# Kernel tuning notes

Hardware: AMD Instinct MI355X
Metric: run time of the kernel (lower is better)

## Reference

```python
import jax, jax.numpy as jnp
import numpy as np

N = 100000
E = 800000
HID = 128
HEADS = 4
HD = HID // HEADS  # 32
EPS_SOFTMAX = 1e-16
LN_EPS = 1e-5


def setup_inputs() -> dict:
    key = jax.random.key(0)
    ks = jax.random.split(key, 12)
    s = 1.0 / np.sqrt(HID)
    x = jax.random.normal(ks[0], (N, HID), dtype=jnp.float32)
    edge_index = jax.random.randint(ks[1], (2, E), 0, N, dtype=jnp.int64)
    Wq = jax.random.normal(ks[2], (HID, HID), dtype=jnp.float32) * s
    bq = jnp.zeros((HID,), jnp.float32)
    Wk = jax.random.normal(ks[3], (HID, HID), dtype=jnp.float32) * s
    bk = jnp.zeros((HID,), jnp.float32)
    Wv = jax.random.normal(ks[4], (HID, HID), dtype=jnp.float32) * s
    bv = jnp.zeros((HID,), jnp.float32)
    Ws = jax.random.normal(ks[5], (HID, HID), dtype=jnp.float32) * s
    bs = jnp.zeros((HID,), jnp.float32)
    gamma = jnp.ones((HID,), jnp.float32)
    beta = jnp.zeros((HID,), jnp.float32)
    return {"x": x, "edge_index": edge_index, "Wq": Wq, "bq": bq,
            "Wk": Wk, "bk": bk, "Wv": Wv, "bv": bv,
            "Ws": Ws, "bs": bs, "gamma": gamma, "beta": beta}


def _transformer_conv(x, edge_index, Wq, bq, Wk, bk, Wv, bv, Ws, bs, gamma, beta):
    src = edge_index[0]  # message source j
    dst = edge_index[1]  # message target i
    # Projections -> [N, HEADS, HD]
    q = (x @ Wq + bq).reshape(N, HEADS, HD)
    k = (x @ Wk + bk).reshape(N, HEADS, HD)
    v = (x @ Wv + bv).reshape(N, HEADS, HD)
    # Edge-wise attention logits [E, HEADS]
    alpha = jnp.einsum('ehd,ehd->eh', q[dst], k[src]) / np.sqrt(HD).astype(np.float32)
    # Segment (per-destination) softmax, numerically stable
    amax = jax.ops.segment_max(alpha, dst, num_segments=N)  # [N, HEADS]
    amax = jnp.where(jnp.isfinite(amax), amax, 0.0)
    ex = jnp.exp(alpha - amax[dst])
    denom = jax.ops.segment_sum(ex, dst, num_segments=N)
    alpha = ex / (denom[dst] + EPS_SOFTMAX)
    # Weighted scatter-add of values
    out = jax.ops.segment_sum(alpha[:, :, None] * v[src], dst, num_segments=N)
    out = out.reshape(N, HID)
    # Root/skip connection (PyG root_weight=True, concat=True)
    out = out + x @ Ws + bs
    # LayerNorm
    mu = jnp.mean(out, axis=-1, keepdims=True)
    var = jnp.mean(jnp.square(out - mu), axis=-1, keepdims=True)
    return (out - mu) * jax.lax.rsqrt(var + LN_EPS) * gamma + beta


def reference(x, edge_index, Wq, bq, Wk, bk, Wv, bv, Ws, bs, gamma, beta):
    return _transformer_conv(x, edge_index, Wq, bq, Wk, bk, Wv, bv, Ws, bs, gamma, beta)
```

## Files before the change

kernel.cpp:

```cpp
#include <hip/hip_runtime.h>
#include <math.h>

#define N_NODES 100000
#define N_EDGES 800000
#define HID 128
#define HEADS 4
#define HD 32

#define KSCALE_L2E 0.2550348554422384f

#define PROJ_BLOCKS 391
#define FILL_BLOCKS 1563

typedef __attribute__((ext_vector_type(8))) short short8;
typedef __attribute__((ext_vector_type(4))) float f32x4;
typedef _Float16 h2 __attribute__((ext_vector_type(2)));
typedef __fp16 hf2 __attribute__((ext_vector_type(2)));

__device__ __forceinline__ unsigned int f2bf(float f) {
    unsigned int u = __float_as_uint(f);
    u += 0x7FFFu + ((u >> 16) & 1u);
    return (u >> 16) & 0xFFFFu;
}
__device__ __forceinline__ h2 u2h(unsigned int u) { return __builtin_bit_cast(h2, u); }
__device__ __forceinline__ unsigned int h2u(h2 h) { return __builtin_bit_cast(unsigned int, h); }
__device__ __forceinline__ unsigned int h2u(hf2 h) { return __builtin_bit_cast(unsigned int, h); }

__global__ __launch_bounds__(256) void prep(
    const float* __restrict__ Wq, const float* __restrict__ Wk,
    const float* __restrict__ Wv, const float* __restrict__ Ws,
    uint4* __restrict__ wtbf, const int* __restrict__ ei,
    int* __restrict__ deg)
{
    const int b = blockIdx.x;
    if (b < 32) {
        int idx = b * 256 + threadIdx.x;
        int m = idx >> 11, n = (idx >> 4) & 127, kc = idx & 15;
        const float* W = (m == 0) ? Wq : (m == 1) ? Wk : (m == 2) ? Wv : Ws;
        unsigned int h[8];
        #pragma unroll
        for (int j = 0; j < 8; ++j) h[j] = f2bf(W[(kc * 8 + j) * HID + n]);
        uint4 o;
        o.x = h[0] | (h[1] << 16);
        o.y = h[2] | (h[3] << 16);
        o.z = h[4] | (h[5] << 16);
        o.w = h[6] | (h[7] << 16);
        wtbf[idx] = o;
    } else {
        int e = (b - 32) * 256 + threadIdx.x;
        if (e < N_EDGES) atomicAdd(&deg[ei[N_EDGES + e]], 1);
    }
}

__global__ __launch_bounds__(256) void scan_local(const int* __restrict__ deg,
                                                  int* __restrict__ rowptr,
                                                  int* __restrict__ bsum)
{
    __shared__ int wsums[4];
    const int b = blockIdx.x, t = threadIdx.x, lane = t & 63, wid = t >> 6;
    const int base = b * 2048 + t * 8;
    int v[8], s = 0;
    #pragma unroll
    for (int j = 0; j < 8; ++j) {
        int i = base + j;
        v[j] = (i < N_NODES) ? deg[i] : 0;
        s += v[j];
    }
    const int tsum = s;
    int x = tsum;
    #pragma unroll
    for (int off = 1; off < 64; off <<= 1) {
        int t2 = __shfl_up(x, off);
        if (lane >= off) x += t2;
    }
    if (lane == 63) wsums[wid] = x;
    __syncthreads();
    int wpre = 0;
    #pragma unroll
    for (int ww = 0; ww < 4; ++ww) { if (ww < wid) wpre += wsums[ww]; }
    int run = wpre + x - tsum;
    #pragma unroll
    for (int j = 0; j < 8; ++j) {
        int i = base + j;
        if (i < N_NODES) rowptr[i] = run;
        run += v[j];
    }
    if (t == 0) bsum[b] = wsums[0] + wsums[1] + wsums[2] + wsums[3];
}

__global__ __launch_bounds__(256) void add_off(int* __restrict__ rowptr,
                                               const int* __restrict__ bsum)
{
    __shared__ int offs;
    const int t = threadIdx.x;
    const int tgt = blockIdx.x >> 3;
    if (t < 64) {
        int v = (t < tgt) ? bsum[t] : 0;
        #pragma unroll
        for (int off = 1; off < 64; off <<= 1) v += __shfl_xor(v, off);
        if (t == 0) offs = v;
    }
    __syncthreads();
    int i = blockIdx.x * 256 + t;
    if (i < N_NODES) rowptr[i] += offs;
    if (blockIdx.x == 0 && t == 0) rowptr[N_NODES] = N_EDGES;
}

__global__ __launch_bounds__(512) void fill_proj(
    const int* __restrict__ ei, const int* __restrict__ rowptr,
    int* __restrict__ deg, int* __restrict__ csr_src,
    const float* __restrict__ x, const uint4* __restrict__ wtbf,
    const float* __restrict__ bq, const float* __restrict__ bk,
    const float* __restrict__ bv, const float* __restrict__ bs,
    unsigned short* __restrict__ Qh, unsigned short* __restrict__ KVh,
    unsigned short* __restrict__ Sh)
{
    __shared__ uint4 wt[4096];

    if (blockIdx.x >= PROJ_BLOCKS) {
        int e = (blockIdx.x - PROJ_BLOCKS) * 512 + threadIdx.x;
        if (e < N_EDGES) {
            int src = ei[e], dst = ei[N_EDGES + e];
            int old = atomicSub(&deg[dst], 1);
            csr_src[rowptr[dst] + old - 1] = src;
        }
        return;
    }

    const int rb   = blockIdx.x * 256;
    const int tid  = threadIdx.x;
    const int lane = tid & 63;
    const int w    = tid >> 6;
    const int r    = lane & 15;
    const int kg   = lane >> 4;

    const int grow0 = rb + w * 32 + r;
    const int grow1 = grow0 + 16;
    short8 afr[2][4];
    #pragma unroll
    for (int rg = 0; rg < 2; ++rg) {
        const int grow = rg ? grow1 : grow0;
        #pragma unroll
        for (int s = 0; s < 4; ++s) {
            float4 a = make_float4(0.f, 0.f, 0.f, 0.f);
            float4 b = make_float4(0.f, 0.f, 0.f, 0.f);
            if (grow < N_NODES) {
                const float4* p = (const float4*)(x + (size_t)grow * HID + (s * 4 + kg) * 8);
                a = p[0]; b = p[1];
            }
            uint4 o;
            o.x = f2bf(a.x) | (f2bf(a.y) << 16);
            o.y = f2bf(a.z) | (f2bf(a.w) << 16);
            o.z = f2bf(b.x) | (f2bf(b.y) << 16);
            o.w = f2bf(b.z) | (f2bf(b.w) << 16);
            afr[rg][s] = *(short8*)&o;
        }
    }

    #pragma unroll
    for (int pair = 0; pair < 2; ++pair) {
        if (pair == 1) __syncthreads();
        #pragma unroll
        for (int it = 0; it < 8; ++it) {
            int cid = it * 512 + tid;
            int kc = cid & 15, n = (cid >> 4) & 127;
            wt[(cid & ~15) | (kc ^ (n & 7))] = wtbf[pair * 4096 + cid];
        }
        __syncthreads();

        #pragma unroll
        for (int mh = 0; mh < 2; ++mh) {
            const int m = pair * 2 + mh;
            const float* bias = (m == 0) ? bq : (m == 1) ? bk : (m == 2) ? bv : bs;
            const uint4* wtm = wt + mh * 2048;
            #pragma unroll
            for (int nt = 0; nt < 8; ++nt) {
                const int nrow = nt * 16 + r;
                const uint4* wrow = wtm + nrow * 16;
                f32x4 acc0, acc1;
                acc0[0]=0.f; acc0[1]=0.f; acc0[2]=0.f; acc0[3]=0.f;
                acc1[0]=0.f; acc1[1]=0.f; acc1[2]=0.f; acc1[3]=0.f;
                #pragma unroll
                for (int s = 0; s < 4; ++s) {
                    short8 bfr = *(const short8*)&wrow[(s * 4 + kg) ^ (nrow & 7)];
                    acc0 = __builtin_amdgcn_mfma_f32_16x16x32_bf16(bfr, afr[0][s], acc0, 0, 0, 0);
                    acc1 = __builtin_amdgcn_mfma_f32_16x16x32_bf16(bfr, afr[1][s], acc1, 0, 0, 0);
                }
                const int col = nt * 16 + kg * 4;
                float4 bi = *(const float4*)(bias + col);
                #pragma unroll
                for (int rg = 0; rg < 2; ++rg) {
                    const int grow = rg ? grow1 : grow0;
                    if (grow < N_NODES) {
                        f32x4 acc = rg ? acc1 : acc0;
                        float vx = acc[0] + bi.x, vy = acc[1] + bi.y;
                        float vz = acc[2] + bi.z, vw = acc[3] + bi.w;
                        if (m == 1) { vx *= KSCALE_L2E; vy *= KSCALE_L2E;
                                      vz *= KSCALE_L2E; vw *= KSCALE_L2E; }
                        uint2 pk;
                        pk.x = h2u(__builtin_amdgcn_cvt_pkrtz(vx, vy));
                        pk.y = h2u(__builtin_amdgcn_cvt_pkrtz(vz, vw));
                        unsigned short* dst =
                            (m == 0) ? (Qh + (size_t)grow * HID + col) :
                            (m == 1) ? (KVh + (size_t)grow * 256 + col) :
                            (m == 2) ? (KVh + (size_t)grow * 256 + 128 + col) :
                                       (Sh + (size_t)grow * HID + col);
                        *(uint2*)dst = pk;
                    }
                }
            }
        }
    }
}

__global__ __launch_bounds__(256) void node_attn(
    const int* __restrict__ rowptr, const int* __restrict__ csr_src,
    const unsigned short* __restrict__ Qh, const unsigned short* __restrict__ KVh,
    const unsigned short* __restrict__ Sh,
    const float* __restrict__ gamma, const float* __restrict__ beta,
    float* __restrict__ out)
{
    const int tid  = threadIdx.x;
    const int lane = tid & 63;
    const int node = blockIdx.x * 4 + (tid >> 6);
    if (node >= N_NODES) return;

    const int l8  = lane & 7;
    const int sl  = lane >> 3;
    const int j16 = l8 * 16;

    const int r0 = rowptr[node], r1 = rowptr[node + 1];

    const uint4* qp = (const uint4*)(Qh + (size_t)node * HID + j16);
    uint4 qa = qp[0], qb = qp[1];
    const h2 q0 = u2h(qa.x), q1 = u2h(qa.y), q2 = u2h(qa.z), q3 = u2h(qa.w);
    const h2 q4 = u2h(qb.x), q5 = u2h(qb.y), q6 = u2h(qb.z), q7 = u2h(qb.w);

    float den = 0.f;
    h2 ac0 = {0,0}, ac1 = {0,0}, ac2 = {0,0}, ac3 = {0,0};
    h2 ac4 = {0,0}, ac5 = {0,0}, ac6 = {0,0}, ac7 = {0,0};

    int p = r0 + sl;
    uint4 ka = {0,0,0,0}, kb = {0,0,0,0}, va = {0,0,0,0}, vb = {0,0,0,0};
    if (p < r1) {
        const unsigned short* base = KVh + (size_t)csr_src[p] * 256 + j16;
        ka = *(const uint4*)(base);
        kb = *(const uint4*)(base + 8);
        va = *(const uint4*)(base + 128);
        vb = *(const uint4*)(base + 136);
    }

    for (int it = r0; it < r1; it += 8) {
        uint4 kan = {0,0,0,0}, kbn = {0,0,0,0}, van = {0,0,0,0}, vbn = {0,0,0,0};
        const int pn = p + 8;
        if (pn < r1) {
            const unsigned short* base = KVh + (size_t)csr_src[pn] * 256 + j16;
            kan = *(const uint4*)(base);
            kbn = *(const uint4*)(base + 8);
            van = *(const uint4*)(base + 128);
            vbn = *(const uint4*)(base + 136);
        }

        h2 d = q0 * u2h(ka.x);
        d += q1 * u2h(ka.y);
        d += q2 * u2h(ka.z);
        d += q3 * u2h(ka.w);
        d += q4 * u2h(kb.x);
        d += q5 * u2h(kb.y);
        d += q6 * u2h(kb.z);
        d += q7 * u2h(kb.w);
        float t = (float)d.x + (float)d.y;
        t += __shfl_xor(t, 1);

        float e = (p < r1) ? __builtin_amdgcn_exp2f(t) : 0.f;
        den += e;
        _Float16 eh = (_Float16)e;
        h2 e2 = {eh, eh};
        ac0 += e2 * u2h(va.x);
        ac1 += e2 * u2h(va.y);
        ac2 += e2 * u2h(va.z);
        ac3 += e2 * u2h(va.w);
        ac4 += e2 * u2h(vb.x);
        ac5 += e2 * u2h(vb.y);
        ac6 += e2 * u2h(vb.z);
        ac7 += e2 * u2h(vb.w);

        p = pn; ka = kan; kb = kbn; va = van; vb = vbn;
    }

    #pragma unroll
    for (int msk = 8; msk <= 32; msk <<= 1) {
        den += __shfl_xor(den, msk);
        ac0 += u2h(__shfl_xor(h2u(ac0), msk));
        ac1 += u2h(__shfl_xor(h2u(ac1), msk));
        ac2 += u2h(__shfl_xor(h2u(ac2), msk));
        ac3 += u2h(__shfl_xor(h2u(ac3), msk));
        ac4 += u2h(__shfl_xor(h2u(ac4), msk));
        ac5 += u2h(__shfl_xor(h2u(ac5), msk));
        ac6 += u2h(__shfl_xor(h2u(ac6), msk));
        ac7 += u2h(__shfl_xor(h2u(ac7), msk));
    }

    float inv = 1.0f / (den + 1e-16f);
    const uint4* spp = (const uint4*)(Sh + (size_t)node * HID + j16);
    uint4 sa = spp[0], sb = spp[1];
    const h2 s0 = u2h(sa.x), s1 = u2h(sa.y), s2 = u2h(sa.z), s3 = u2h(sa.w);
    const h2 s4 = u2h(sb.x), s5 = u2h(sb.y), s6 = u2h(sb.z), s7 = u2h(sb.w);

    float o[16];
    o[0]  = (float)ac0.x * inv + (float)s0.x;  o[1]  = (float)ac0.y * inv + (float)s0.y;
    o[2]  = (float)ac1.x * inv + (float)s1.x;  o[3]  = (float)ac1.y * inv + (float)s1.y;
    o[4]  = (float)ac2.x * inv + (float)s2.x;  o[5]  = (float)ac2.y * inv + (float)s2.y;
    o[6]  = (float)ac3.x * inv + (float)s3.x;  o[7]  = (float)ac3.y * inv + (float)s3.y;
    o[8]  = (float)ac4.x * inv + (float)s4.x;  o[9]  = (float)ac4.y * inv + (float)s4.y;
    o[10] = (float)ac5.x * inv + (float)s5.x;  o[11] = (float)ac5.y * inv + (float)s5.y;
    o[12] = (float)ac6.x * inv + (float)s6.x;  o[13] = (float)ac6.y * inv + (float)s6.y;
    o[14] = (float)ac7.x * inv + (float)s7.x;  o[15] = (float)ac7.y * inv + (float)s7.y;

    float sum = 0.f, sq = 0.f;
    #pragma unroll
    for (int i = 0; i < 16; ++i) { sum += o[i]; sq += o[i] * o[i]; }
    #pragma unroll
    for (int off = 1; off < 8; off <<= 1) {
        sum += __shfl_xor(sum, off);
        sq  += __shfl_xor(sq, off);
    }
    float mean = sum * (1.0f / 128.0f);
    float var  = sq * (1.0f / 128.0f) - mean * mean;
    float rstd = rsqrtf(var + 1e-5f);

    if (sl == 0) {
        float* op = out + (size_t)node * HID + j16;
        #pragma unroll
        for (int c = 0; c < 4; ++c) {
            float4 g = *(const float4*)(gamma + j16 + c * 4);
            float4 b = *(const float4*)(beta + j16 + c * 4);
            float4 wv;
            wv.x = (o[c*4+0] - mean) * rstd * g.x + b.x;
            wv.y = (o[c*4+1] - mean) * rstd * g.y + b.y;
            wv.z = (o[c*4+2] - mean) * rstd * g.z + b.z;
            wv.w = (o[c*4+3] - mean) * rstd * g.w + b.w;
            *(float4*)(op + c * 4) = wv;
        }
    }
}

extern "C" void kernel_launch(void* const* d_in, const int* in_sizes, int n_in,
                              void* d_out, int out_size, void* d_ws, size_t ws_size,
                              hipStream_t stream) {
    const float* x  = (const float*)d_in[0];
    const int*   ei = (const int*)d_in[1];
    const float* Wq = (const float*)d_in[2];
    const float* bq = (const float*)d_in[3];
    const float* Wk = (const float*)d_in[4];
    const float* bk = (const float*)d_in[5];
    const float* Wv = (const float*)d_in[6];
    const float* bv = (const float*)d_in[7];
    const float* Ws = (const float*)d_in[8];
    const float* bs = (const float*)d_in[9];
    const float* gamma = (const float*)d_in[10];
    const float* beta  = (const float*)d_in[11];
    float* out = (float*)d_out;

    unsigned short* Qh  = (unsigned short*)d_ws;
    unsigned short* KVh = Qh + (size_t)N_NODES * HID;
    unsigned short* Sh  = KVh + (size_t)N_NODES * 256;
    uint4* wtbf  = (uint4*)(Sh + (size_t)N_NODES * HID);
    int* deg     = (int*)(wtbf + 4 * 128 * 16);
    int* rowptr  = deg + N_NODES;
    int* csr_src = rowptr + (N_NODES + 1);
    int* bsum    = csr_src + N_EDGES;

    hipMemsetAsync(deg, 0, N_NODES * sizeof(int), stream);

    const int eblk = (N_EDGES + 255) / 256;
    prep<<<32 + eblk, 256, 0, stream>>>(Wq, Wk, Wv, Ws, wtbf, ei, deg);

    const int nb = (N_NODES + 2047) / 2048;
    scan_local<<<nb, 256, 0, stream>>>(deg, rowptr, bsum);
    add_off<<<(N_NODES + 255) / 256, 256, 0, stream>>>(rowptr, bsum);

    fill_proj<<<PROJ_BLOCKS + FILL_BLOCKS, 512, 0, stream>>>(
        ei, rowptr, deg, csr_src, x, wtbf, bq, bk, bv, bs, Qh, KVh, Sh);

    node_attn<<<(N_NODES + 3) / 4, 256, 0, stream>>>(rowptr, csr_src, Qh, KVh, Sh,
                                                     gamma, beta, out);
}
```

Before: 197.0 us.

## Split fused CSR fill and projection into separate kernels, halve weight LDS

The combined fill_proj kernel is split into a standalone csr_fill kernel (256 threads per edge block) and a proj_mfma kernel. The projection kernel now stages one weight matrix at a time (32 KB of LDS instead of 64 KB), looping four times with a barrier between matrices. This is meant to raise occupancy for the projection blocks. The cost is an extra kernel launch, more barriers, and losing the overlap of edge scatter with the MFMA work inside a single grid.

```diff
diff --git a/kernel.cpp b/kernel.cpp
--- a/kernel.cpp
+++ b/kernel.cpp
@@ -8,9 +8,6 @@
 #define HD 32
 
 #define KSCALE_L2E 0.2550348554422384f
-
-#define PROJ_BLOCKS 391
-#define FILL_BLOCKS 1563
 
 typedef __attribute__((ext_vector_type(8))) short short8;
 typedef __attribute__((ext_vector_type(4))) float f32x4;
@@ -106,26 +103,26 @@
     if (blockIdx.x == 0 && t == 0) rowptr[N_NODES] = N_EDGES;
 }
 
-__global__ __launch_bounds__(512) void fill_proj(
-    const int* __restrict__ ei, const int* __restrict__ rowptr,
-    int* __restrict__ deg, int* __restrict__ csr_src,
+__global__ __launch_bounds__(256) void csr_fill(const int* __restrict__ ei,
+                                                const int* __restrict__ rowptr,
+                                                int* __restrict__ deg,
+                                                int* __restrict__ csr_src)
+{
+    int e = blockIdx.x * 256 + threadIdx.x;
+    if (e >= N_EDGES) return;
+    int src = ei[e], dst = ei[N_EDGES + e];
+    int old = atomicSub(&deg[dst], 1);
+    csr_src[rowptr[dst] + old - 1] = src;
+}
+
+__global__ __launch_bounds__(512) void proj_mfma(
     const float* __restrict__ x, const uint4* __restrict__ wtbf,
     const float* __restrict__ bq, const float* __restrict__ bk,
     const float* __restrict__ bv, const float* __restrict__ bs,
     unsigned short* __restrict__ Qh, unsigned short* __restrict__ KVh,
     unsigned short* __restrict__ Sh)
 {
-    __shared__ uint4 wt[4096];
-
-    if (blockIdx.x >= PROJ_BLOCKS) {
-        int e = (blockIdx.x - PROJ_BLOCKS) * 512 + threadIdx.x;
-        if (e < N_EDGES) {
-            int src = ei[e], dst = ei[N_EDGES + e];
-            int old = atomicSub(&deg[dst], 1);
-            csr_src[rowptr[dst] + old - 1] = src;
-        }
-        return;
-    }
+    __shared__ uint4 wt[2048];
 
     const int rb   = blockIdx.x * 256;
     const int tid  = threadIdx.x;
@@ -158,55 +155,50 @@
     }
 
     #pragma unroll
-    for (int pair = 0; pair < 2; ++pair) {
-        if (pair == 1) __syncthreads();
-        #pragma unroll
-        for (int it = 0; it < 8; ++it) {
+    for (int m = 0; m < 4; ++m) {
+        if (m > 0) __syncthreads();
+        #pragma unroll
+        for (int it = 0; it < 4; ++it) {
             int cid = it * 512 + tid;
             int kc = cid & 15, n = (cid >> 4) & 127;
-            wt[(cid & ~15) | (kc ^ (n & 7))] = wtbf[pair * 4096 + cid];
+            wt[(cid & ~15) | (kc ^ (n & 7))] = wtbf[m * 2048 + cid];
         }
         __syncthreads();
 
-        #pragma unroll
-        for (int mh = 0; mh < 2; ++mh) {
-            const int m = pair * 2 + mh;
-            const float* bias = (m == 0) ? bq : (m == 1) ? bk : (m == 2) ? bv : bs;
-            const uint4* wtm = wt + mh * 2048;
+        const float* bias = (m == 0) ? bq : (m == 1) ? bk : (m == 2) ? bv : bs;
+        #pragma unroll
+        for (int nt = 0; nt < 8; ++nt) {
+            const int nrow = nt * 16 + r;
+            const uint4* wrow = wt + nrow * 16;
+            f32x4 acc0, acc1;
+            acc0[0]=0.f; acc0[1]=0.f; acc0[2]=0.f; acc0[3]=0.f;
+            acc1[0]=0.f; acc1[1]=0.f; acc1[2]=0.f; acc1[3]=0.f;
             #pragma unroll
-            for (int nt = 0; nt < 8; ++nt) {
-                const int nrow = nt * 16 + r;
-                const uint4* wrow = wtm + nrow * 16;
-                f32x4 acc0, acc1;
-                acc0[0]=0.f; acc0[1]=0.f; acc0[2]=0.f; acc0[3]=0.f;
-                acc1[0]=0.f; acc1[1]=0.f; acc1[2]=0.f; acc1[3]=0.f;
-                #pragma unroll
-                for (int s = 0; s < 4; ++s) {
-                    short8 bfr = *(const short8*)&wrow[(s * 4 + kg) ^ (nrow & 7)];
-                    acc0 = __builtin_amdgcn_mfma_f32_16x16x32_bf16(bfr, afr[0][s], acc0, 0, 0, 0);
-                    acc1 = __builtin_amdgcn_mfma_f32_16x16x32_bf16(bfr, afr[1][s], acc1, 0, 0, 0);
-                }
-                const int col = nt * 16 + kg * 4;
-                float4 bi = *(const float4*)(bias + col);
-                #pragma unroll
-                for (int rg = 0; rg < 2; ++rg) {
-                    const int grow = rg ? grow1 : grow0;
-                    if (grow < N_NODES) {
-                        f32x4 acc = rg ? acc1 : acc0;
-                        float vx = acc[0] + bi.x, vy = acc[1] + bi.y;
-                        float vz = acc[2] + bi.z, vw = acc[3] + bi.w;
-                        if (m == 1) { vx *= KSCALE_L2E; vy *= KSCALE_L2E;
-                                      vz *= KSCALE_L2E; vw *= KSCALE_L2E; }
-                        uint2 pk;
-                        pk.x = h2u(__builtin_amdgcn_cvt_pkrtz(vx, vy));
-                        pk.y = h2u(__builtin_amdgcn_cvt_pkrtz(vz, vw));
-                        unsigned short* dst =
-                            (m == 0) ? (Qh + (size_t)grow * HID + col) :
-                            (m == 1) ? (KVh + (size_t)grow * 256 + col) :
-                            (m == 2) ? (KVh + (size_t)grow * 256 + 128 + col) :
-                                       (Sh + (size_t)grow * HID + col);
-                        *(uint2*)dst = pk;
-                    }
+            for (int s = 0; s < 4; ++s) {
+                short8 bfr = *(const short8*)&wrow[(s * 4 + kg) ^ (nrow & 7)];
+                acc0 = __builtin_amdgcn_mfma_f32_16x16x32_bf16(bfr, afr[0][s], acc0, 0, 0, 0);
+                acc1 = __builtin_amdgcn_mfma_f32_16x16x32_bf16(bfr, afr[1][s], acc1, 0, 0, 0);
+            }
+            const int col = nt * 16 + kg * 4;
+            float4 bi = *(const float4*)(bias + col);
+            #pragma unroll
+            for (int rg = 0; rg < 2; ++rg) {
+                const int grow = rg ? grow1 : grow0;
+                if (grow < N_NODES) {
+                    f32x4 acc = rg ? acc1 : acc0;
+                    float vx = acc[0] + bi.x, vy = acc[1] + bi.y;
+                    float vz = acc[2] + bi.z, vw = acc[3] + bi.w;
+                    if (m == 1) { vx *= KSCALE_L2E; vy *= KSCALE_L2E;
+                                  vz *= KSCALE_L2E; vw *= KSCALE_L2E; }
+                    uint2 pk;
+                    pk.x = h2u(__builtin_amdgcn_cvt_pkrtz(vx, vy));
+                    pk.y = h2u(__builtin_amdgcn_cvt_pkrtz(vz, vw));
+                    unsigned short* dst =
+                        (m == 0) ? (Qh + (size_t)grow * HID + col) :
+                        (m == 1) ? (KVh + (size_t)grow * 256 + col) :
+                        (m == 2) ? (KVh + (size_t)grow * 256 + 128 + col) :
+                                   (Sh + (size_t)grow * HID + col);
+                    *(uint2*)dst = pk;
                 }
             }
         }
@@ -379,9 +371,11 @@
     const int nb = (N_NODES + 2047) / 2048;
     scan_local<<<nb, 256, 0, stream>>>(deg, rowptr, bsum);
     add_off<<<(N_NODES + 255) / 256, 256, 0, stream>>>(rowptr, bsum);
-
-    fill_proj<<<PROJ_BLOCKS + FILL_BLOCKS, 512, 0, stream>>>(
-        ei, rowptr, deg, csr_src, x, wtbf, bq, bk, bv, bs, Qh, KVh, Sh);
+    csr_fill<<<eblk, 256, 0, stream>>>(ei, rowptr, deg, csr_src);
+
+    const int row_tiles = (N_NODES + 255) / 256;
+    proj_mfma<<<row_tiles, 512, 0, stream>>>(x, wtbf, bq, bk, bv, bs,
+                                             Qh, KVh, Sh);
 
     node_attn<<<(N_NODES + 3) / 4, 256, 0, stream>>>(rowptr, csr_src, Qh, KVh, Sh,
                                                      gamma, beta, out);
```

New measurement: 217.5 us. 10.4% more time.
